# Kernel optimization log

Measured on AMD Instinct MI355X. Metric: run time of the kernel, lower is better.

The kernel has to match this reference:

```python
import jax, jax.numpy as jnp
import numpy as np

N_HEAD = 16
TEMPERATURE = 1.0

def setup_inputs() -> dict:
    key = jax.random.key(0)
    ks = jax.random.split(key, 5)
    B, L, D = 2, 2048, 1024
    s = 0.02
    return {
        'x':     jax.random.normal(ks[0], (B, L, D), jnp.float32),
        'q_g':   jax.random.normal(ks[1], (B, L, D), jnp.float32),
        'k_g':   jax.random.normal(ks[2], (B, L, D), jnp.float32),
        'W_qkv': jax.random.normal(ks[3], (D, 3 * D), jnp.float32) * s,
        'W_out': jax.random.normal(ks[4], (D, D), jnp.float32) * s,
    }

def reference(x, q_g, k_g, W_qkv, W_out):
    B, L, D = x.shape
    H = N_HEAD
    hd = D // H
    qkv = x @ W_qkv                                    # [B, L, 3D]
    q, k, v = jnp.split(qkv, 3, axis=-1)
    def to_heads(t):                                    # [B,L,D] -> [B,H,L,hd]
        return t.reshape(B, L, H, hd).transpose(0, 2, 1, 3)
    q, k, v = to_heads(q), to_heads(k), to_heads(v)
    qg, kg = to_heads(q_g), to_heads(k_g)

    scale = 1.0 / jnp.sqrt(jnp.float32(hd))
    # dual score matrices (same math as concat-on-head-dim then split)
    aw_x = jnp.einsum('bhqd,bhkd->bhqk', q, k) * scale    # [B,H,L,L]
    aw_g = jnp.einsum('bhqd,bhkd->bhqk', qg, kg) * scale  # [B,H,L,L]
    # sensory_attention=True, merge='add'
    attn = aw_x + aw_g

    causal = jnp.tril(jnp.ones((L, L), dtype=bool))
    attn = jnp.where(causal, attn, -jnp.inf)
    log_norm = jnp.log(jnp.float32(L))                    # softmax_log_norm=True
    attn = jax.nn.softmax(attn / (log_norm * TEMPERATURE), axis=-1)

    y = jnp.einsum('bhqk,bhkd->bhqd', attn, v)            # [B,H,L,hd]
    y = y.transpose(0, 2, 1, 3).reshape(B, L, D)
    return y @ W_out
```

## Files before the change

kernel.cpp:

```cpp
#include <hip/hip_runtime.h>
#include <type_traits>

typedef __attribute__((ext_vector_type(8))) short bf16x8;
typedef __attribute__((ext_vector_type(4))) float f32x4;

static __device__ __forceinline__ unsigned short f2bf(float f) {
    unsigned int u = __float_as_uint(f);
    u += 0x7fffu + ((u >> 16) & 1u);
    return (unsigned short)(u >> 16);
}
static __device__ __forceinline__ unsigned int pack2bf(float lo, float hi) {
    return ((__float_as_uint(lo) + 0x8000u) >> 16) |
           ((__float_as_uint(hi) + 0x8000u) & 0xffff0000u);
}

static __device__ __forceinline__ float bf2f(short v) {
    return __uint_as_float(((unsigned int)(unsigned short)v) << 16);
}

static __device__ __forceinline__ bf16x8 cvt8v(const float* p) {
    f32x4 a = *(const f32x4*)p, b = *(const f32x4*)(p + 4);
    bf16x8 r;
    r[0] = (short)f2bf(a[0]); r[1] = (short)f2bf(a[1]);
    r[2] = (short)f2bf(a[2]); r[3] = (short)f2bf(a[3]);
    r[4] = (short)f2bf(b[0]); r[5] = (short)f2bf(b[1]);
    r[6] = (short)f2bf(b[2]); r[7] = (short)f2bf(b[3]);
    return r;
}
static __device__ __forceinline__ bf16x8 scale8v(bf16x8 v, float s) {
    bf16x8 r;
    #pragma unroll
    for (int j = 0; j < 8; ++j) r[j] = (short)f2bf(bf2f(v[j]) * s);
    return r;
}
static __device__ __forceinline__ uint4 cvt8(const float* p) {
    bf16x8 r = cvt8v(p);
    union { bf16x8 v; uint4 u; } c; c.v = r; return c.u;
}

static __device__ __forceinline__ void glds16(const unsigned short* g, unsigned short* l) {
    __builtin_amdgcn_global_load_lds(
        (const __attribute__((address_space(1))) unsigned int*)g,
        (__attribute__((address_space(3))) unsigned int*)l, 16, 0, 0);
}

__global__ __launch_bounds__(256) void cvt_bf16_2(
    const float* __restrict__ a, unsigned short* __restrict__ da,
    const float* __restrict__ b, unsigned short* __restrict__ db)
{
    int i = blockIdx.x * 256 + threadIdx.x;
    const float* s = (i < 524288) ? a : b;
    unsigned short* d = (i < 524288) ? da : db;
    size_t j = (size_t)((i < 524288) ? i : i - 524288) * 8;
    *(uint4*)&d[j] = cvt8(&s[j]);
}

__global__ __launch_bounds__(256) void transpose_cvt(
    const float* __restrict__ src, unsigned short* __restrict__ dst, int R, int C)
{
    __shared__ unsigned short t[64 * 72];
    const int r0 = blockIdx.y * 64, c0 = blockIdx.x * 64;
    const int tid = threadIdx.x;
    #pragma unroll
    for (int i = 0; i < 4; ++i) {
        int idx = tid + i * 256;
        int row = idx >> 4, seg = idx & 15;
        f32x4 v = *(const f32x4*)&src[(size_t)(r0 + row) * C + c0 + seg * 4];
        #pragma unroll
        for (int j = 0; j < 4; ++j) t[row * 72 + seg * 4 + j] = f2bf(v[j]);
    }
    __syncthreads();
    #pragma unroll
    for (int i = 0; i < 2; ++i) {
        int idx = tid + i * 256;
        int row = idx >> 3, seg = idx & 7;
        uint4 tv; unsigned short* tmp = (unsigned short*)&tv;
        #pragma unroll
        for (int j = 0; j < 8; ++j) tmp[j] = t[(seg * 8 + j) * 72 + row];
        *(uint4*)&dst[(size_t)(c0 + row) * R + r0 + seg * 8] = tv;
    }
}

__global__ __launch_bounds__(256) void transpose_v(
    const unsigned short* __restrict__ qkv, unsigned short* __restrict__ vt)
{
    __shared__ unsigned short t[64 * 72];
    const int lt = blockIdx.x, bh = blockIdx.y, b = bh >> 4, h = bh & 15;
    const int tid = threadIdx.x;
    #pragma unroll
    for (int i = 0; i < 2; ++i) {
        int idx = tid + i * 256, row = idx >> 3, seg = idx & 7;
        *(uint4*)&t[row * 72 + seg * 8] =
            *(const uint4*)&qkv[(size_t)(b * 2048 + lt * 64 + row) * 3072 + 2048 + h * 64 + seg * 8];
    }
    __syncthreads();
    #pragma unroll
    for (int i = 0; i < 2; ++i) {
        int idx = tid + i * 256, row = idx >> 3, seg = idx & 7;
        uint4 tv; unsigned short* tmp = (unsigned short*)&tv;
        #pragma unroll
        for (int j = 0; j < 8; ++j) tmp[j] = t[(seg * 8 + j) * 72 + row];
        *(uint4*)&vt[((size_t)bh * 64 + row) * 2048 + lt * 64 + seg * 8] = tv;
    }
}

template <typename OT>
__global__ __launch_bounds__(256) void gemm_lds(
    const unsigned short* __restrict__ A, const unsigned short* __restrict__ Bt,
    OT* __restrict__ C, int M, int N, int K)
{
    __shared__ unsigned short As[128 * 32];
    __shared__ unsigned short Bs[128 * 32];
    const int tid = threadIdx.x;
    const int wave = tid >> 6, lane = tid & 63, quad = lane >> 4, l16 = lane & 15;
    const int wr = (wave >> 1) * 64, wc = (wave & 1) * 64;
    const int m0 = blockIdx.y * 128, n0 = blockIdx.x * 128;

    const unsigned short* ga = A  + (size_t)(m0 + wave * 32 + (lane >> 2)) * K + (lane & 3) * 8;
    const unsigned short* gb = Bt + (size_t)(n0 + wave * 32 + (lane >> 2)) * K + (lane & 3) * 8;
    unsigned short* la = &As[wave * 32 * 32];
    unsigned short* lb = &Bs[wave * 32 * 32];
    const size_t step16 = (size_t)16 * K;

    f32x4 acc[4][4];
    #pragma unroll
    for (int i = 0; i < 4; ++i)
        #pragma unroll
        for (int j = 0; j < 4; ++j) acc[i][j] = (f32x4){0.f, 0.f, 0.f, 0.f};

    for (int kt = 0; kt < K; kt += 32) {
        glds16(ga, la);
        glds16(ga + step16, la + 512);
        glds16(gb, lb);
        glds16(gb + step16, lb + 512);
        ga += 32; gb += 32;
        __syncthreads();
        bf16x8 af[4], bf[4];
        #pragma unroll
        for (int i = 0; i < 4; ++i) {
            af[i] = *(const bf16x8*)&As[(wr + i * 16 + l16) * 32 + quad * 8];
            bf[i] = *(const bf16x8*)&Bs[(wc + i * 16 + l16) * 32 + quad * 8];
        }
        #pragma unroll
        for (int mi = 0; mi < 4; ++mi)
            #pragma unroll
            for (int ni = 0; ni < 4; ++ni)
                acc[mi][ni] = __builtin_amdgcn_mfma_f32_16x16x32_bf16(
                    af[mi], bf[ni], acc[mi][ni], 0, 0, 0);
        __syncthreads();
    }
    #pragma unroll
    for (int mi = 0; mi < 4; ++mi)
        #pragma unroll
        for (int ni = 0; ni < 4; ++ni)
            #pragma unroll
            for (int r = 0; r < 4; ++r) {
                int row = m0 + wr + mi * 16 + quad * 4 + r;
                int col = n0 + wc + ni * 16 + l16;
                if constexpr (std::is_same_v<OT, float>)
                    C[(size_t)row * N + col] = acc[mi][ni][r];
                else
                    C[(size_t)row * N + col] = f2bf(acc[mi][ni][r]);
            }
}

__global__ __launch_bounds__(256, 4) void attn6(
    const unsigned short* __restrict__ qkv, const float* __restrict__ qg,
    const unsigned short* __restrict__ kgb, const unsigned short* __restrict__ vt,
    unsigned short* __restrict__ y)
{
    const int L = 2048, D3 = 3072, Dm = 1024;
    const float SC2 = 0.125f * 1.44269504088896f / 7.6246189861593985f;

    const int qt = 31 - (int)blockIdx.y;
    const int bh = blockIdx.x, b = bh >> 4, h = bh & 15;
    const int tid = threadIdx.x, wave = tid >> 6, lane = tid & 63;
    const int quad = lane >> 4, l16 = lane & 15;

    __shared__ unsigned short K_l[4096];
    __shared__ unsigned short G_l[4096];
    __shared__ unsigned short V_l[4096];
    __shared__ unsigned short P_l[4 * 1152];
    unsigned short* Pw = &P_l[wave * 1152];

    bf16x8 qf[2], gf[2];
    {
        const int qrow = qt * 64 + wave * 16 + l16;
        const unsigned short* qp = qkv + (size_t)(b * L + qrow) * D3 + h * 64;
        const float* gp = qg + (size_t)(b * L + qrow) * Dm + h * 64;
        #pragma unroll
        for (int c = 0; c < 2; ++c) {
            qf[c] = scale8v(*(const bf16x8*)(qp + c * 32 + quad * 8), SC2);
            gf[c] = scale8v(cvt8v(gp + c * 32 + quad * 8), SC2);
        }
    }

    f32x4 o[4];
    #pragma unroll
    for (int nd = 0; nd < 4; ++nd) o[nd] = (f32x4){0.f, 0.f, 0.f, 0.f};
    float lsum = 0.f;

    const int srow = wave * 16 + (lane >> 3);
    const int c8 = (((lane & 7) ^ (lane >> 3)) & 7) * 8;
    const unsigned short* pk = qkv + (size_t)(b * L + srow) * D3 + 1024 + h * 64 + c8;
    const unsigned short* pg = kgb + (size_t)(b * L + srow) * Dm + h * 64 + c8;
    const unsigned short* pv = vt + ((size_t)bh * 64 + srow) * L + c8;
    unsigned short* lK = &K_l[wave * 1024];
    unsigned short* lG = &G_l[wave * 1024];
    unsigned short* lV = &V_l[wave * 1024];

    const int rb = l16 * 128;
    const int swz0 = ((quad     ^ (l16 & 7)) * 16);
    const int swz1 = (((4 + quad) ^ (l16 & 7)) * 16);

    for (int kt = 0; kt < qt; ++kt) {
        __syncthreads();
        glds16(pk, lK); glds16(pk + 8 * D3, lK + 512);
        glds16(pg, lG); glds16(pg + 8 * Dm, lG + 512);
        glds16(pv, lV); glds16(pv + 8 * L,  lV + 512);
        pk += 64 * D3; pg += 64 * Dm; pv += 64;
        __syncthreads();

        #pragma unroll
        for (int ni = 0; ni < 4; ++ni) {
            bf16x8 kf0 = *(const bf16x8*)((const char*)K_l + rb + swz0 + ni * 2048);
            bf16x8 kf1 = *(const bf16x8*)((const char*)K_l + rb + swz1 + ni * 2048);
            bf16x8 gb0 = *(const bf16x8*)((const char*)G_l + rb + swz0 + ni * 2048);
            bf16x8 gb1 = *(const bf16x8*)((const char*)G_l + rb + swz1 + ni * 2048);
            f32x4 a = (f32x4){0.f, 0.f, 0.f, 0.f};
            a = __builtin_amdgcn_mfma_f32_16x16x32_bf16(kf0, qf[0], a, 0, 0, 0);
            a = __builtin_amdgcn_mfma_f32_16x16x32_bf16(gb0, gf[0], a, 0, 0, 0);
            a = __builtin_amdgcn_mfma_f32_16x16x32_bf16(kf1, qf[1], a, 0, 0, 0);
            a = __builtin_amdgcn_mfma_f32_16x16x32_bf16(gb1, gf[1], a, 0, 0, 0);
            float e0 = exp2f(a[0]), e1 = exp2f(a[1]);
            float e2 = exp2f(a[2]), e3 = exp2f(a[3]);
            lsum += (e0 + e1) + (e2 + e3);
            unsigned int p01 = pack2bf(e0, e1), p23 = pack2bf(e2, e3);
            *(unsigned long long*)&Pw[l16 * 72 + ni * 16 + quad * 4] =
                ((unsigned long long)p23 << 32) | p01;
        }
        asm volatile("s_waitcnt lgkmcnt(0)" ::: "memory");

        bf16x8 pa[2];
        #pragma unroll
        for (int c = 0; c < 2; ++c)
            pa[c] = *(const bf16x8*)&Pw[l16 * 72 + c * 32 + quad * 8];
        #pragma unroll
        for (int nd = 0; nd < 4; ++nd) {
            bf16x8 vf0 = *(const bf16x8*)((const char*)V_l + rb + swz0 + nd * 2048);
            bf16x8 vf1 = *(const bf16x8*)((const char*)V_l + rb + swz1 + nd * 2048);
            o[nd] = __builtin_amdgcn_mfma_f32_16x16x32_bf16(pa[0], vf0, o[nd], 0, 0, 0);
            o[nd] = __builtin_amdgcn_mfma_f32_16x16x32_bf16(pa[1], vf1, o[nd], 0, 0, 0);
        }
    }

    {
        __syncthreads();
        glds16(pk, lK); glds16(pk + 8 * D3, lK + 512);
        glds16(pg, lG); glds16(pg + 8 * Dm, lG + 512);
        glds16(pv, lV); glds16(pv + 8 * L,  lV + 512);
        __syncthreads();

        #pragma unroll
        for (int ni = 0; ni < 4; ++ni) {
            if (ni > wave) {
                *(unsigned long long*)&Pw[l16 * 72 + ni * 16 + quad * 4] = 0ull;
                continue;
            }
            bf16x8 kf0 = *(const bf16x8*)((const char*)K_l + rb + swz0 + ni * 2048);
            bf16x8 kf1 = *(const bf16x8*)((const char*)K_l + rb + swz1 + ni * 2048);
            bf16x8 gb0 = *(const bf16x8*)((const char*)G_l + rb + swz0 + ni * 2048);
            bf16x8 gb1 = *(const bf16x8*)((const char*)G_l + rb + swz1 + ni * 2048);
            f32x4 a = (f32x4){0.f, 0.f, 0.f, 0.f};
            a = __builtin_amdgcn_mfma_f32_16x16x32_bf16(kf0, qf[0], a, 0, 0, 0);
            a = __builtin_amdgcn_mfma_f32_16x16x32_bf16(gb0, gf[0], a, 0, 0, 0);
            a = __builtin_amdgcn_mfma_f32_16x16x32_bf16(kf1, qf[1], a, 0, 0, 0);
            a = __builtin_amdgcn_mfma_f32_16x16x32_bf16(gb1, gf[1], a, 0, 0, 0);
            float e0, e1, e2, e3;
            if (ni < wave) {
                e0 = exp2f(a[0]); e1 = exp2f(a[1]);
                e2 = exp2f(a[2]); e3 = exp2f(a[3]);
            } else {
                e0 = (quad * 4 + 0 <= l16) ? exp2f(a[0]) : 0.f;
                e1 = (quad * 4 + 1 <= l16) ? exp2f(a[1]) : 0.f;
                e2 = (quad * 4 + 2 <= l16) ? exp2f(a[2]) : 0.f;
                e3 = (quad * 4 + 3 <= l16) ? exp2f(a[3]) : 0.f;
            }
            lsum += (e0 + e1) + (e2 + e3);
            unsigned int p01 = pack2bf(e0, e1), p23 = pack2bf(e2, e3);
            *(unsigned long long*)&Pw[l16 * 72 + ni * 16 + quad * 4] =
                ((unsigned long long)p23 << 32) | p01;
        }
        asm volatile("s_waitcnt lgkmcnt(0)" ::: "memory");

        bf16x8 pa[2];
        #pragma unroll
        for (int c = 0; c < 2; ++c)
            pa[c] = *(const bf16x8*)&Pw[l16 * 72 + c * 32 + quad * 8];
        #pragma unroll
        for (int nd = 0; nd < 4; ++nd) {
            bf16x8 vf0 = *(const bf16x8*)((const char*)V_l + rb + swz0 + nd * 2048);
            bf16x8 vf1 = *(const bf16x8*)((const char*)V_l + rb + swz1 + nd * 2048);
            o[nd] = __builtin_amdgcn_mfma_f32_16x16x32_bf16(pa[0], vf0, o[nd], 0, 0, 0);
            o[nd] = __builtin_amdgcn_mfma_f32_16x16x32_bf16(pa[1], vf1, o[nd], 0, 0, 0);
        }
    }

    float rs = lsum;
    rs += __shfl_xor(rs, 16);
    rs += __shfl_xor(rs, 32);
    #pragma unroll
    for (int r = 0; r < 4; ++r) {
        float inv = 1.f / __shfl(rs, (lane & 48) | (quad * 4 + r));
        int row = qt * 64 + wave * 16 + quad * 4 + r;
        #pragma unroll
        for (int nd = 0; nd < 4; ++nd)
            y[(size_t)(b * L + row) * Dm + h * 64 + nd * 16 + l16] =
                f2bf(o[nd][r] * inv);
    }
}

extern "C" void kernel_launch(void* const* d_in, const int* in_sizes, int n_in,
                              void* d_out, int out_size, void* d_ws, size_t ws_size,
                              hipStream_t stream) {
    const float* x     = (const float*)d_in[0];
    const float* q_g   = (const float*)d_in[1];
    const float* k_g   = (const float*)d_in[2];
    const float* W_qkv = (const float*)d_in[3];
    const float* W_out = (const float*)d_in[4];
    float* out = (float*)d_out;
    unsigned short* ws = (unsigned short*)d_ws;

    unsigned short* qkv_ws = ws;
    unsigned short* y_ws   = ws + 12582912;
    unsigned short* wtq    = ws + 16777216;
    unsigned short* wto    = ws + 19922944;
    unsigned short* kg_bf  = ws + 20971520;
    unsigned short* x_bf   = ws + 25165824;
    unsigned short* vt_bf  = x_bf;

    dim3 blk(256);
    cvt_bf16_2<<<4096, blk, 0, stream>>>(x, x_bf, k_g, kg_bf);
    transpose_cvt<<<dim3(48, 16), blk, 0, stream>>>(W_qkv, wtq, 1024, 3072);
    transpose_cvt<<<dim3(16, 16), blk, 0, stream>>>(W_out, wto, 1024, 1024);
    gemm_lds<unsigned short><<<dim3(24, 32), blk, 0, stream>>>(
        x_bf, wtq, qkv_ws, 4096, 3072, 1024);
    transpose_v<<<dim3(32, 32), blk, 0, stream>>>(qkv_ws, vt_bf);
    attn6<<<dim3(32, 32), blk, 0, stream>>>(qkv_ws, q_g, kg_bf, vt_bf, y_ws);
    gemm_lds<float><<<dim3(8, 32), blk, 0, stream>>>(
        y_ws, wto, out, 4096, 1024, 1024);
}
```

Measured before the change: 233.3 us.

## Fuse prep kernels, write V transposed from QKV GEMM, retile out-proj, swizzle P

Merges the three conversion/transpose kernels into one prep_all launch. The QKV GEMM now writes V directly in transposed per-head layout through an LDS staging buffer, which removes the separate transpose_v kernel. The output projection uses a 128x64 tile to put more blocks on the grid. Attention replaces the padded P buffer with an XOR-swizzled layout that uses less LDS, and raises the occupancy hint to 5 blocks. Risks are the extra LDS in gemm_qkv lowering its occupancy, and register pressure at the higher launch bound.

Result: faster. 225.6 us (-3.3%).

```diff
diff --git a/kernel.cpp b/kernel.cpp
--- a/kernel.cpp
+++ b/kernel.cpp
@@ -1,5 +1,4 @@
 #include <hip/hip_runtime.h>
-#include <type_traits>
 
 typedef __attribute__((ext_vector_type(8))) short bf16x8;
 typedef __attribute__((ext_vector_type(4))) float f32x4;
@@ -13,11 +12,9 @@
     return ((__float_as_uint(lo) + 0x8000u) >> 16) |
            ((__float_as_uint(hi) + 0x8000u) & 0xffff0000u);
 }
-
 static __device__ __forceinline__ float bf2f(short v) {
     return __uint_as_float(((unsigned int)(unsigned short)v) << 16);
 }
-
 static __device__ __forceinline__ bf16x8 cvt8v(const float* p) {
     f32x4 a = *(const f32x4*)p, b = *(const f32x4*)(p + 4);
     bf16x8 r;
@@ -37,30 +34,18 @@
     bf16x8 r = cvt8v(p);
     union { bf16x8 v; uint4 u; } c; c.v = r; return c.u;
 }
-
 static __device__ __forceinline__ void glds16(const unsigned short* g, unsigned short* l) {
     __builtin_amdgcn_global_load_lds(
         (const __attribute__((address_space(1))) unsigned int*)g,
         (__attribute__((address_space(3))) unsigned int*)l, 16, 0, 0);
 }
 
-__global__ __launch_bounds__(256) void cvt_bf16_2(
-    const float* __restrict__ a, unsigned short* __restrict__ da,
-    const float* __restrict__ b, unsigned short* __restrict__ db)
-{
-    int i = blockIdx.x * 256 + threadIdx.x;
-    const float* s = (i < 524288) ? a : b;
-    unsigned short* d = (i < 524288) ? da : db;
-    size_t j = (size_t)((i < 524288) ? i : i - 524288) * 8;
-    *(uint4*)&d[j] = cvt8(&s[j]);
-}
-
-__global__ __launch_bounds__(256) void transpose_cvt(
-    const float* __restrict__ src, unsigned short* __restrict__ dst, int R, int C)
+static __device__ __forceinline__ void transpose_tile(
+    const float* __restrict__ src, unsigned short* __restrict__ dst,
+    int R, int C, int bx, int by, int tid)
 {
     __shared__ unsigned short t[64 * 72];
-    const int r0 = blockIdx.y * 64, c0 = blockIdx.x * 64;
-    const int tid = threadIdx.x;
+    const int r0 = by * 64, c0 = bx * 64;
     #pragma unroll
     for (int i = 0; i < 4; ++i) {
         int idx = tid + i * 256;
@@ -81,36 +66,36 @@
     }
 }
 
-__global__ __launch_bounds__(256) void transpose_v(
-    const unsigned short* __restrict__ qkv, unsigned short* __restrict__ vt)
+__global__ __launch_bounds__(256) void prep_all(
+    const float* __restrict__ x, unsigned short* __restrict__ x_bf,
+    const float* __restrict__ kg, unsigned short* __restrict__ kg_bf,
+    const float* __restrict__ Wq, unsigned short* __restrict__ wtq,
+    const float* __restrict__ Wo, unsigned short* __restrict__ wto)
 {
-    __shared__ unsigned short t[64 * 72];
-    const int lt = blockIdx.x, bh = blockIdx.y, b = bh >> 4, h = bh & 15;
-    const int tid = threadIdx.x;
-    #pragma unroll
-    for (int i = 0; i < 2; ++i) {
-        int idx = tid + i * 256, row = idx >> 3, seg = idx & 7;
-        *(uint4*)&t[row * 72 + seg * 8] =
-            *(const uint4*)&qkv[(size_t)(b * 2048 + lt * 64 + row) * 3072 + 2048 + h * 64 + seg * 8];
-    }
-    __syncthreads();
-    #pragma unroll
-    for (int i = 0; i < 2; ++i) {
-        int idx = tid + i * 256, row = idx >> 3, seg = idx & 7;
-        uint4 tv; unsigned short* tmp = (unsigned short*)&tv;
-        #pragma unroll
-        for (int j = 0; j < 8; ++j) tmp[j] = t[(seg * 8 + j) * 72 + row];
-        *(uint4*)&vt[((size_t)bh * 64 + row) * 2048 + lt * 64 + seg * 8] = tv;
-    }
-}
-
-template <typename OT>
-__global__ __launch_bounds__(256) void gemm_lds(
+    const int t = blockIdx.x, tid = threadIdx.x;
+    if (t < 2048) {
+        size_t j = ((size_t)t * 256 + tid) * 8;
+        *(uint4*)&x_bf[j] = cvt8(&x[j]);
+    } else if (t < 4096) {
+        size_t j = ((size_t)(t - 2048) * 256 + tid) * 8;
+        *(uint4*)&kg_bf[j] = cvt8(&kg[j]);
+    } else if (t < 4864) {
+        int tt = t - 4096;
+        transpose_tile(Wq, wtq, 1024, 3072, tt % 48, tt / 48, tid);
+    } else {
+        int tt = t - 4864;
+        transpose_tile(Wo, wto, 1024, 1024, tt & 15, tt >> 4, tid);
+    }
+}
+
+__global__ __launch_bounds__(256) void gemm_qkv(
     const unsigned short* __restrict__ A, const unsigned short* __restrict__ Bt,
-    OT* __restrict__ C, int M, int N, int K)
+    unsigned short* __restrict__ qk, unsigned short* __restrict__ vt)
 {
+    const int K = 1024;
     __shared__ unsigned short As[128 * 32];
     __shared__ unsigned short Bs[128 * 32];
+    __shared__ unsigned short Tb[128 * 136];
     const int tid = threadIdx.x;
     const int wave = tid >> 6, lane = tid & 63, quad = lane >> 4, l16 = lane & 15;
     const int wr = (wave >> 1) * 64, wc = (wave & 1) * 64;
@@ -129,10 +114,8 @@
         for (int j = 0; j < 4; ++j) acc[i][j] = (f32x4){0.f, 0.f, 0.f, 0.f};
 
     for (int kt = 0; kt < K; kt += 32) {
-        glds16(ga, la);
-        glds16(ga + step16, la + 512);
-        glds16(gb, lb);
-        glds16(gb + step16, lb + 512);
+        glds16(ga, la); glds16(ga + step16, la + 512);
+        glds16(gb, lb); glds16(gb + step16, lb + 512);
         ga += 32; gb += 32;
         __syncthreads();
         bf16x8 af[4], bf[4];
@@ -149,27 +132,102 @@
                     af[mi], bf[ni], acc[mi][ni], 0, 0, 0);
         __syncthreads();
     }
+
+    if (blockIdx.x < 16) {
+        #pragma unroll
+        for (int mi = 0; mi < 4; ++mi)
+            #pragma unroll
+            for (int ni = 0; ni < 4; ++ni)
+                #pragma unroll
+                for (int r = 0; r < 4; ++r) {
+                    int row = m0 + wr + mi * 16 + quad * 4 + r;
+                    int col = n0 + wc + ni * 16 + l16;
+                    qk[(size_t)row * 2048 + col] = f2bf(acc[mi][ni][r]);
+                }
+    } else {
+        __syncthreads();
+        #pragma unroll
+        for (int mi = 0; mi < 4; ++mi)
+            #pragma unroll
+            for (int ni = 0; ni < 4; ++ni)
+                #pragma unroll
+                for (int r = 0; r < 4; ++r) {
+                    int col = wc + ni * 16 + l16;
+                    int row = wr + mi * 16 + quad * 4 + r;
+                    Tb[col * 136 + row] = f2bf(acc[mi][ni][r]);
+                }
+        __syncthreads();
+        const int col = tid >> 1, r0 = (tid & 1) * 64;
+        const int bh = (m0 >> 11) * 16 + ((int)blockIdx.x - 16) * 2 + (col >> 6);
+        size_t base = ((size_t)bh * 64 + (col & 63)) * 2048 + (m0 & 2047) + r0;
+        #pragma unroll
+        for (int k = 0; k < 8; ++k)
+            *(uint4*)&vt[base + k * 8] = *(const uint4*)&Tb[col * 136 + r0 + k * 8];
+    }
+}
+
+__global__ __launch_bounds__(256) void gemm_n64(
+    const unsigned short* __restrict__ A, const unsigned short* __restrict__ Bt,
+    float* __restrict__ C)
+{
+    const int K = 1024, N = 1024;
+    __shared__ unsigned short As[128 * 32];
+    __shared__ unsigned short Bs[64 * 32];
+    const int tid = threadIdx.x;
+    const int wave = tid >> 6, lane = tid & 63, quad = lane >> 4, l16 = lane & 15;
+    const int wr = (wave >> 1) * 64, wc = (wave & 1) * 32;
+    const int m0 = blockIdx.y * 128, n0 = blockIdx.x * 64;
+
+    const unsigned short* ga = A  + (size_t)(m0 + wave * 32 + (lane >> 2)) * K + (lane & 3) * 8;
+    const unsigned short* gb = Bt + (size_t)(n0 + wave * 16 + (lane >> 2)) * K + (lane & 3) * 8;
+    unsigned short* la = &As[wave * 32 * 32];
+    unsigned short* lb = &Bs[wave * 16 * 32];
+    const size_t step16 = (size_t)16 * K;
+
+    f32x4 acc[4][2];
+    #pragma unroll
+    for (int i = 0; i < 4; ++i)
+        #pragma unroll
+        for (int j = 0; j < 2; ++j) acc[i][j] = (f32x4){0.f, 0.f, 0.f, 0.f};
+
+    for (int kt = 0; kt < K; kt += 32) {
+        glds16(ga, la); glds16(ga + step16, la + 512);
+        glds16(gb, lb);
+        ga += 32; gb += 32;
+        __syncthreads();
+        bf16x8 af[4], bf[2];
+        #pragma unroll
+        for (int i = 0; i < 4; ++i)
+            af[i] = *(const bf16x8*)&As[(wr + i * 16 + l16) * 32 + quad * 8];
+        #pragma unroll
+        for (int i = 0; i < 2; ++i)
+            bf[i] = *(const bf16x8*)&Bs[(wc + i * 16 + l16) * 32 + quad * 8];
+        #pragma unroll
+        for (int mi = 0; mi < 4; ++mi)
+            #pragma unroll
+            for (int ni = 0; ni < 2; ++ni)
+                acc[mi][ni] = __builtin_amdgcn_mfma_f32_16x16x32_bf16(
+                    af[mi], bf[ni], acc[mi][ni], 0, 0, 0);
+        __syncthreads();
+    }
     #pragma unroll
     for (int mi = 0; mi < 4; ++mi)
         #pragma unroll
-        for (int ni = 0; ni < 4; ++ni)
+        for (int ni = 0; ni < 2; ++ni)
             #pragma unroll
             for (int r = 0; r < 4; ++r) {
                 int row = m0 + wr + mi * 16 + quad * 4 + r;
                 int col = n0 + wc + ni * 16 + l16;
-                if constexpr (std::is_same_v<OT, float>)
-                    C[(size_t)row * N + col] = acc[mi][ni][r];
-                else
-                    C[(size_t)row * N + col] = f2bf(acc[mi][ni][r]);
+                C[(size_t)row * N + col] = acc[mi][ni][r];
             }
 }
 
-__global__ __launch_bounds__(256, 4) void attn6(
-    const unsigned short* __restrict__ qkv, const float* __restrict__ qg,
+__global__ __launch_bounds__(256, 5) void attn7(
+    const unsigned short* __restrict__ qk, const float* __restrict__ qg,
     const unsigned short* __restrict__ kgb, const unsigned short* __restrict__ vt,
     unsigned short* __restrict__ y)
 {
-    const int L = 2048, D3 = 3072, Dm = 1024;
+    const int L = 2048, DS = 2048, Dm = 1024;
     const float SC2 = 0.125f * 1.44269504088896f / 7.6246189861593985f;
 
     const int qt = 31 - (int)blockIdx.y;
@@ -180,13 +238,13 @@
     __shared__ unsigned short K_l[4096];
     __shared__ unsigned short G_l[4096];
     __shared__ unsigned short V_l[4096];
-    __shared__ unsigned short P_l[4 * 1152];
-    unsigned short* Pw = &P_l[wave * 1152];
+    __shared__ unsigned short P_l[4096];
+    unsigned short* Pw = &P_l[wave * 1024];
 
     bf16x8 qf[2], gf[2];
     {
         const int qrow = qt * 64 + wave * 16 + l16;
-        const unsigned short* qp = qkv + (size_t)(b * L + qrow) * D3 + h * 64;
+        const unsigned short* qp = qk + (size_t)(b * L + qrow) * DS + h * 64;
         const float* gp = qg + (size_t)(b * L + qrow) * Dm + h * 64;
         #pragma unroll
         for (int c = 0; c < 2; ++c) {
@@ -202,7 +260,7 @@
 
     const int srow = wave * 16 + (lane >> 3);
     const int c8 = (((lane & 7) ^ (lane >> 3)) & 7) * 8;
-    const unsigned short* pk = qkv + (size_t)(b * L + srow) * D3 + 1024 + h * 64 + c8;
+    const unsigned short* pk = qk + (size_t)(b * L + srow) * DS + 1024 + h * 64 + c8;
     const unsigned short* pg = kgb + (size_t)(b * L + srow) * Dm + h * 64 + c8;
     const unsigned short* pv = vt + ((size_t)bh * 64 + srow) * L + c8;
     unsigned short* lK = &K_l[wave * 1024];
@@ -212,13 +270,15 @@
     const int rb = l16 * 128;
     const int swz0 = ((quad     ^ (l16 & 7)) * 16);
     const int swz1 = (((4 + quad) ^ (l16 & 7)) * 16);
+    const int pwb = l16 * 64 + (quad & 1) * 4;
+    const int pwc = quad >> 1, pxr = l16 & 7;
 
     for (int kt = 0; kt < qt; ++kt) {
         __syncthreads();
-        glds16(pk, lK); glds16(pk + 8 * D3, lK + 512);
+        glds16(pk, lK); glds16(pk + 8 * DS, lK + 512);
         glds16(pg, lG); glds16(pg + 8 * Dm, lG + 512);
         glds16(pv, lV); glds16(pv + 8 * L,  lV + 512);
-        pk += 64 * D3; pg += 64 * Dm; pv += 64;
+        pk += 64 * DS; pg += 64 * Dm; pv += 64;
         __syncthreads();
 
         #pragma unroll
@@ -236,7 +296,7 @@
             float e2 = exp2f(a[2]), e3 = exp2f(a[3]);
             lsum += (e0 + e1) + (e2 + e3);
             unsigned int p01 = pack2bf(e0, e1), p23 = pack2bf(e2, e3);
-            *(unsigned long long*)&Pw[l16 * 72 + ni * 16 + quad * 4] =
+            *(unsigned long long*)&Pw[pwb + (((ni * 2 + pwc) ^ pxr) * 8)] =
                 ((unsigned long long)p23 << 32) | p01;
         }
         asm volatile("s_waitcnt lgkmcnt(0)" ::: "memory");
@@ -244,7 +304,7 @@
         bf16x8 pa[2];
         #pragma unroll
         for (int c = 0; c < 2; ++c)
-            pa[c] = *(const bf16x8*)&Pw[l16 * 72 + c * 32 + quad * 8];
+            pa[c] = *(const bf16x8*)&Pw[l16 * 64 + (((c * 4 + quad) ^ pxr) * 8)];
         #pragma unroll
         for (int nd = 0; nd < 4; ++nd) {
             bf16x8 vf0 = *(const bf16x8*)((const char*)V_l + rb + swz0 + nd * 2048);
@@ -256,7 +316,7 @@
 
     {
         __syncthreads();
-        glds16(pk, lK); glds16(pk + 8 * D3, lK + 512);
+        glds16(pk, lK); glds16(pk + 8 * DS, lK + 512);
         glds16(pg, lG); glds16(pg + 8 * Dm, lG + 512);
         glds16(pv, lV); glds16(pv + 8 * L,  lV + 512);
         __syncthreads();
@@ -264,7 +324,7 @@
         #pragma unroll
         for (int ni = 0; ni < 4; ++ni) {
             if (ni > wave) {
-                *(unsigned long long*)&Pw[l16 * 72 + ni * 16 + quad * 4] = 0ull;
+                *(unsigned long long*)&Pw[pwb + (((ni * 2 + pwc) ^ pxr) * 8)] = 0ull;
                 continue;
             }
             bf16x8 kf0 = *(const bf16x8*)((const char*)K_l + rb + swz0 + ni * 2048);
@@ -288,7 +348,7 @@
             }
             lsum += (e0 + e1) + (e2 + e3);
             unsigned int p01 = pack2bf(e0, e1), p23 = pack2bf(e2, e3);
-            *(unsigned long long*)&Pw[l16 * 72 + ni * 16 + quad * 4] =
+            *(unsigned long long*)&Pw[pwb + (((ni * 2 + pwc) ^ pxr) * 8)] =
                 ((unsigned long long)p23 << 32) | p01;
         }
         asm volatile("s_waitcnt lgkmcnt(0)" ::: "memory");
@@ -296,7 +356,7 @@
         bf16x8 pa[2];
         #pragma unroll
         for (int c = 0; c < 2; ++c)
-            pa[c] = *(const bf16x8*)&Pw[l16 * 72 + c * 32 + quad * 8];
+            pa[c] = *(const bf16x8*)&Pw[l16 * 64 + (((c * 4 + quad) ^ pxr) * 8)];
         #pragma unroll
         for (int nd = 0; nd < 4; ++nd) {
             bf16x8 vf0 = *(const bf16x8*)((const char*)V_l + rb + swz0 + nd * 2048);
@@ -331,22 +391,17 @@
     float* out = (float*)d_out;
     unsigned short* ws = (unsigned short*)d_ws;
 
-    unsigned short* qkv_ws = ws;
-    unsigned short* y_ws   = ws + 12582912;
-    unsigned short* wtq    = ws + 16777216;
-    unsigned short* wto    = ws + 19922944;
-    unsigned short* kg_bf  = ws + 20971520;
-    unsigned short* x_bf   = ws + 25165824;
-    unsigned short* vt_bf  = x_bf;
+    unsigned short* qk_ws = ws;
+    unsigned short* y_ws  = ws + 8388608;
+    unsigned short* wtq   = ws + 12582912;
+    unsigned short* wto   = ws + 15728640;
+    unsigned short* kg_bf = ws + 16777216;
+    unsigned short* x_bf  = ws + 20971520;
+    unsigned short* vt_bf = ws + 25165824;
 
     dim3 blk(256);
-    cvt_bf16_2<<<4096, blk, 0, stream>>>(x, x_bf, k_g, kg_bf);
-    transpose_cvt<<<dim3(48, 16), blk, 0, stream>>>(W_qkv, wtq, 1024, 3072);
-    transpose_cvt<<<dim3(16, 16), blk, 0, stream>>>(W_out, wto, 1024, 1024);
-    gemm_lds<unsigned short><<<dim3(24, 32), blk, 0, stream>>>(
-        x_bf, wtq, qkv_ws, 4096, 3072, 1024);
-    transpose_v<<<dim3(32, 32), blk, 0, stream>>>(qkv_ws, vt_bf);
-    attn6<<<dim3(32, 32), blk, 0, stream>>>(qkv_ws, q_g, kg_bf, vt_bf, y_ws);
-    gemm_lds<float><<<dim3(8, 32), blk, 0, stream>>>(
-        y_ws, wto, out, 4096, 1024, 1024);
-}
+    prep_all<<<5120, blk, 0, stream>>>(x, x_bf, k_g, kg_bf, W_qkv, wtq, W_out, wto);
+    gemm_qkv<<<dim3(24, 32), blk, 0, stream>>>(x_bf, wtq, qk_ws, vt_bf);
+    attn7<<<dim3(32, 32), blk, 0, stream>>>(qk_ws, q_g, kg_bf, vt_bf, y_ws);
+    gemm_n64<<<dim3(16, 32), blk, 0, stream>>>(y_ws, wto, out);
+}
```
